# Optimization experiments

Measured on AMD Instinct MI355X. Metric: run time of the kernel, lower is better.

## Reference

```python
import jax, jax.numpy as jnp
import numpy as np

BETA = 0.25


def setup_inputs() -> dict:
    key = jax.random.key(0)
    k1, k2 = jax.random.split(key)
    x = jax.random.normal(k1, (32, 64, 64, 64), dtype=jnp.float32)   # [B, C, H, W]
    emb = jax.random.normal(k2, (1024, 64), dtype=jnp.float32)       # [K, C] codebook
    return {"x": x, "emb": emb}


def reference(x, emb):
    b, c, h, w = x.shape
    # (b h w) c
    z = jnp.transpose(x, (0, 2, 3, 1)).reshape(-1, c)
    # squared euclidean distances (argmin identical to torch.cdist argmin)
    # ||z||^2 - 2 z e^T + ||e||^2, never taking sqrt since only argmin is used
    d = (jnp.sum(z * z, axis=1, keepdims=True)
         - 2.0 * jnp.einsum('nc,kc->nk', z, emb)
         + jnp.sum(emb * emb, axis=1)[None, :])        # [N, K]
    idx = jnp.argmin(d, axis=1)                        # [N] int
    e = emb[idx]                                       # gather [N, C]
    e = jnp.transpose(e.reshape(b, h, w, c), (0, 3, 1, 2))  # [B, C, H, W]
    codebook_loss = jnp.mean((jax.lax.stop_gradient(x) - e) ** 2)
    commitment_loss = BETA * jnp.mean((x - jax.lax.stop_gradient(e)) ** 2)
    loss = codebook_loss + commitment_loss
    o = x + jax.lax.stop_gradient(e - x)               # straight-through
    indices = idx.reshape(b, h, w)
    return (o, loss, indices)
```

## Files before the change

### kernel.cpp

```cpp
#include <hip/hip_runtime.h>

#define BATCH   32
#define CCH     64
#define HW      4096
#define NPIX    (BATCH * HW)
#define KCODES  1024
#define NELEM   (NPIX * CCH)
#define MB      256
#define CK      64
#define MARGIN_Q 3u

typedef _Float16 f16;
typedef __attribute__((ext_vector_type(8))) _Float16 f16x8;
typedef __attribute__((ext_vector_type(4))) float    f32x4;

static __device__ __forceinline__ f32x4 mfma16(f16x8 a, f16x8 b, f32x4 c) {
    return __builtin_amdgcn_mfma_f32_16x16x32_f16(a, b, c, 0, 0, 0);
}

static __device__ __forceinline__ void dma16(void* lds, const void* g) {
    __builtin_amdgcn_global_load_lds(
        (const __attribute__((address_space(1))) unsigned int*)g,
        (__attribute__((address_space(3))) unsigned int*)lds, 16, 0, 0);
}

static __device__ __forceinline__ unsigned med3u(unsigned a, unsigned b, unsigned c) {
    unsigned d;
    asm("v_med3_u32 %0, %1, %2, %3" : "=v"(d) : "v"(a), "v"(b), "v"(c));
    return d;
}

#define WS_EEB_F   64
#define WS_CBH_B   8192
#define WS_CBL_B   139264
#define WS_WL_U    67584

__global__ __launch_bounds__(256) void vq_prep(
    const float* __restrict__ emb, float* __restrict__ wsf,
    unsigned* __restrict__ wsu, f16* __restrict__ cbH, f16* __restrict__ cbL,
    float* __restrict__ eeb_g)
{
    const int t   = threadIdx.x;
    const int gid = blockIdx.x * 256 + t;
    const int row = gid >> 3, gi = gid & 7;
    if (gid == 0) { wsf[0] = 0.f; wsu[1] = 0u; wsu[2] = 0u; }
    const float* src = emb + (size_t)row * CCH + gi * 8;
    float4 v0 = *(const float4*)(src);
    float4 v1 = *(const float4*)(src + 4);
    float vv[8] = {v0.x, v0.y, v0.z, v0.w, v1.x, v1.y, v1.z, v1.w};
    f16x8 h, l;
    float s = 0.f;
#pragma unroll
    for (int j = 0; j < 8; ++j) {
        f16 hh = (f16)vv[j];
        h[j] = hh;
        l[j] = (f16)(vv[j] - (float)hh);
        s = fmaf(vv[j], vv[j], s);
    }
    const int off = row * 64 + 8 * (gi ^ (row & 7));
    *(f16x8*)(cbH + off) = h;
    *(f16x8*)(cbL + off) = l;
    s += __shfl_xor(s, 1, 64);
    s += __shfl_xor(s, 2, 64);
    s += __shfl_xor(s, 4, 64);
    if (gi == 0) eeb_g[row] = fmaf(s, 2048.0f, 1048576.0f);
}

__global__ __launch_bounds__(512, 4) void vq_main(
    const float* __restrict__ x,
    const float* __restrict__ emb,
    const f16* __restrict__ cbH, const f16* __restrict__ cbL,
    const float* __restrict__ eeb_g,
    float* __restrict__ o, float* __restrict__ idx_out,
    float* __restrict__ acc, unsigned* __restrict__ wl_count,
    unsigned* __restrict__ wl, unsigned cap)
{
    __shared__ __align__(16) char smem[32768];
    __shared__ float eebl[2][CK];
    __shared__ unsigned bu1[MB], bu2[MB];
    __shared__ float wred[8];

    const int t    = threadIdx.x;
    const int lane = t & 63;
    const int w    = t >> 6;
    const int col  = lane & 15;
    const int quad = lane >> 4;
    const int c7   = col & 7;
    const int sw0  = 8 * (quad ^ c7);
    const int sw1  = sw0 ^ 32;
    const int n0   = blockIdx.x * MB;
    const int b    = n0 >> 12;
    const int p0   = n0 & 4095;
    const float* xb = x + (size_t)b * (CCH * HW) + p0;

    auto stage = [&](int chunk, int bufi) {
        const int k0 = chunk * CK;
        char* lb = smem + bufi * 16384;
        const char* gH = (const char*)cbH + (size_t)k0 * 128 + w * 1024 + lane * 16;
        const char* gL = (const char*)cbL + (size_t)k0 * 128 + w * 1024 + lane * 16;
        dma16(lb + w * 1024,        gH);
        dma16(lb + 8192 + w * 1024, gL);
        if (t < CK) eebl[bufi][t] = eeb_g[k0 + t];
    };

    stage(0, 0);

    f16x8 aH[2][2], aL[2][2];
#pragma unroll
    for (int rt = 0; rt < 2; ++rt) {
        const int pp = w * 32 + rt * 16 + col;
#pragma unroll
        for (int kc = 0; kc < 2; ++kc) {
            f16x8 h, l;
#pragma unroll
            for (int j = 0; j < 8; ++j) {
                const int c = kc * 32 + quad * 8 + j;
                float zs = -2.0f * xb[(size_t)c * HW + pp];
                f16 hh = (f16)zs;
                h[j] = hh;
                l[j] = (f16)(zs - (float)hh);
            }
            aH[rt][kc] = h;
            aL[rt][kc] = l;
        }
    }

    unsigned best[8], best2[8];
#pragma unroll
    for (int s = 0; s < 8; ++s) { best[s] = 0xFFFFFFFFu; best2[s] = 0xFFFFFFFFu; }

    const f32x4 zero4 = {0.f, 0.f, 0.f, 0.f};

    for (int chunk = 0; chunk < KCODES / CK; ++chunk) {
        const int cur = chunk & 1;
        __syncthreads();
        if (chunk + 1 < KCODES / CK) stage(chunk + 1, cur ^ 1);

        const f16* bufH = (const f16*)(smem + cur * 16384);
        const f16* bufL = bufH + 4096;
        const int k0 = chunk * CK;

#pragma unroll
        for (int tile = 0; tile < CK / 16; ++tile) {
            const f16* bh = bufH + (tile * 16 + col) * 64;
            const f16* bl = bufL + (tile * 16 + col) * 64;
            f16x8 bH0 = *(const f16x8*)(bh + sw0);
            f16x8 bH1 = *(const f16x8*)(bh + sw1);
            f16x8 bL0 = *(const f16x8*)(bl + sw0);
            f16x8 bL1 = *(const f16x8*)(bl + sw1);
            const float eebc = eebl[cur][tile * 16 + col];
            const unsigned kb = (unsigned)(k0 + tile * 16 + col);
#pragma unroll
            for (int rt = 0; rt < 2; ++rt) {
                f32x4 a4 = mfma16(aH[rt][0], bH0, zero4);
                a4 = mfma16(aH[rt][1], bH1, a4);
                a4 = mfma16(aL[rt][0], bH0, a4);
                a4 = mfma16(aL[rt][1], bH1, a4);
                a4 = mfma16(aH[rt][0], bL0, a4);
                a4 = mfma16(aH[rt][1], bL1, a4);
#pragma unroll
                for (int r = 0; r < 4; ++r) {
                    float uf = fmaf(a4[r], 2048.0f, eebc);
                    unsigned pk = (((unsigned)uf) << 10) | kb;
                    const int s = rt * 4 + r;
                    const unsigned b0 = best[s];
                    best2[s] = med3u(b0, best2[s], pk);
                    best[s]  = min(b0, pk);
                }
            }
        }
    }

#pragma unroll
    for (int d = 1; d < 16; d <<= 1) {
#pragma unroll
        for (int s = 0; s < 8; ++s) {
            unsigned ob  = __shfl_xor(best[s],  d, 64);
            unsigned ob2 = __shfl_xor(best2[s], d, 64);
            best2[s] = min(min(best2[s], ob2), max(best[s], ob));
            best[s]  = min(best[s], ob);
        }
    }
    if (col == 0) {
#pragma unroll
        for (int rt = 0; rt < 2; ++rt)
#pragma unroll
            for (int r = 0; r < 4; ++r) {
                const int pl = w * 32 + rt * 16 + quad * 4 + r;
                bu1[pl] = best[rt * 4 + r];
                bu2[pl] = best2[rt * 4 + r];
            }
    }
    __syncthreads();

    const int pix  = t & 255;
    const int half = t >> 8;
    const unsigned bu = bu1[pix];
    const unsigned bidx = bu & 1023u;
    if (half == 0) {
        idx_out[n0 + t] = (float)bidx;
        const unsigned qg = (bu2[pix] >> 10) - (bu >> 10);
        if (qg < MARGIN_Q) {
            unsigned pos = atomicAdd(wl_count, 1u);
            if (pos < cap) wl[pos] = (unsigned)(n0 + t);
        }
    }
    float ss = 0.f;
    {
        const float4* er4 = (const float4*)(emb + (size_t)bidx * CCH) + half * 8;
        const float* xbt = xb + pix;
        float* ob = o + (size_t)b * (CCH * HW) + p0 + pix;
#pragma unroll
        for (int i = 0; i < 8; ++i) {
            float4 ev = er4[i];
            float evv[4] = {ev.x, ev.y, ev.z, ev.w};
#pragma unroll
            for (int q = 0; q < 4; ++q) {
                const int c = half * 32 + i * 4 + q;
                float xv = xbt[(size_t)c * HW];
                float e  = evv[q];
                ob[(size_t)c * HW] = xv + (e - xv);
                float d = xv - e;
                ss = fmaf(d, d, ss);
            }
        }
    }
    for (int off = 32; off; off >>= 1) ss += __shfl_down(ss, off, 64);
    if (lane == 0) wred[w] = ss;
    __syncthreads();
    if (t == 0) {
        float s2 = 0.f;
#pragma unroll
        for (int q = 0; q < 8; ++q) s2 += wred[q];
        atomicAdd(acc, s2);
    }
}

__global__ __launch_bounds__(256) void vq_refine(
    const float* __restrict__ x, const float* __restrict__ emb,
    float* __restrict__ o, float* __restrict__ idx_out,
    float* __restrict__ acc, const unsigned* __restrict__ wl_count,
    const unsigned* __restrict__ wl, unsigned cap,
    float* __restrict__ loss, unsigned* __restrict__ done)
{
    __shared__ float zsh[CCH];
    __shared__ double rbd[4];
    __shared__ int rbi[4];
    __shared__ int s_pk;
    unsigned cnt = *wl_count; if (cnt > cap) cnt = cap;
    const int t = threadIdx.x;

    for (unsigned i = blockIdx.x; i < cnt; i += gridDim.x) {
        const int n = (int)wl[i];
        const int b = n >> 12, p = n & 4095;
        if (t < CCH) zsh[t] = x[(size_t)b * (CCH * HW) + (size_t)t * HW + p];
        __syncthreads();

        double bd = 1e300; int bi = KCODES;
        for (int j = 0; j < 4; ++j) {
            const int k = t + j * 256;
            const float* er = emb + (size_t)k * CCH;
            double d = 0.0;
#pragma unroll
            for (int c = 0; c < CCH; ++c) {
                double tt = (double)zsh[c] - (double)er[c];
                d = fma(tt, tt, d);
            }
            if (d < bd) { bd = d; bi = k; }
        }
        for (int dlt = 1; dlt < 64; dlt <<= 1) {
            double od = __shfl_xor(bd, dlt, 64);
            int    oi = __shfl_xor(bi, dlt, 64);
            if (od < bd || (od == bd && oi < bi)) { bd = od; bi = oi; }
        }
        const int wv = t >> 6;
        if ((t & 63) == 0) { rbd[wv] = bd; rbi[wv] = bi; }
        __syncthreads();
        if (t == 0) {
            double fb = rbd[0]; int fi = rbi[0];
            for (int q = 1; q < 4; ++q)
                if (rbd[q] < fb || (rbd[q] == fb && rbi[q] < fi)) { fb = rbd[q]; fi = rbi[q]; }
            const int old = (int)idx_out[n];
            if (fi != old) { idx_out[n] = (float)fi; s_pk = (old << 16) | fi; }
            else s_pk = -1;
        }
        __syncthreads();
        const int pk = s_pk;
        if (pk >= 0 && t < CCH) {
            const int old = pk >> 16, fi = pk & 0xFFFF;
            const float xv = zsh[t];
            const float eo = emb[(size_t)old * CCH + t];
            const float en = emb[(size_t)fi  * CCH + t];
            o[(size_t)b * (CCH * HW) + (size_t)t * HW + p] = xv + (en - xv);
            const float dn = xv - en, dd = xv - eo;
            float delta = dn * dn - dd * dd;
            for (int off = 32; off; off >>= 1) delta += __shfl_down(delta, off, 64);
            if (t == 0) atomicAdd(acc, delta);
        }
        __syncthreads();
    }

    __threadfence();
    if (t == 0) {
        unsigned prev = atomicAdd(done, 1u);
        if (prev + 1 == gridDim.x) {
            __threadfence();
            float a = atomicAdd(acc, 0.0f);
            loss[0] = 1.25f * a * (1.0f / (float)NELEM);
        }
    }
}

extern "C" void kernel_launch(void* const* d_in, const int* in_sizes, int n_in,
                              void* d_out, int out_size, void* d_ws, size_t ws_size,
                              hipStream_t stream) {
    const float* x   = (const float*)d_in[0];
    const float* emb = (const float*)d_in[1];
    float*    out = (float*)d_out;
    float*    wsf = (float*)d_ws;
    unsigned* wsu = (unsigned*)d_ws;
    char*     wsb = (char*)d_ws;

    float* o_out    = out;
    float* loss_out = out + NELEM;
    float* idx_out  = out + NELEM + 1;
    float* eeb_g    = wsf + WS_EEB_F;
    f16*   cbH      = (f16*)(wsb + WS_CBH_B);
    f16*   cbL      = (f16*)(wsb + WS_CBL_B);
    unsigned* wl    = wsu + WS_WL_U;
    unsigned cap = 0;
    if (ws_size / 4 > WS_WL_U) {
        size_t c = ws_size / 4 - WS_WL_U;
        cap = (unsigned)(c > NPIX ? NPIX : c);
    }

    vq_prep<<<32, 256, 0, stream>>>(emb, wsf, wsu, cbH, cbL, eeb_g);
    vq_main<<<NPIX / MB, 512, 0, stream>>>(x, emb, cbH, cbL, eeb_g, o_out,
                                           idx_out, wsf, wsu + 1, wl, cap);
    vq_refine<<<512, 256, 0, stream>>>(x, emb, o_out, idx_out, wsf,
                                       wsu + 1, wl, cap, loss_out, wsu + 2);
}
```

Before: 175.6 us.

## Halve pixels per block to raise occupancy and finalize loss in separate kernel

Each vq_main block now handles 128 pixels instead of 256, with each wave processing one 16-row tile instead of two. This halves the A-fragment and best/best2 register state, and the launch bound rises to 8 blocks per CU. The grid doubles, so the codebook is staged through LDS twice as often in total and B-fragment reuse across row tiles is lost. The last-block atomic done-counter in vq_refine is replaced by a tiny separate vq_fin kernel, which adds one extra launch.

```diff
diff --git a/kernel.cpp b/kernel.cpp
--- a/kernel.cpp
+++ b/kernel.cpp
@@ -6,7 +6,7 @@
 #define NPIX    (BATCH * HW)
 #define KCODES  1024
 #define NELEM   (NPIX * CCH)
-#define MB      256
+#define MB      128
 #define CK      64
 #define MARGIN_Q 3u
 
@@ -43,7 +43,7 @@
     const int t   = threadIdx.x;
     const int gid = blockIdx.x * 256 + t;
     const int row = gid >> 3, gi = gid & 7;
-    if (gid == 0) { wsf[0] = 0.f; wsu[1] = 0u; wsu[2] = 0u; }
+    if (gid == 0) { wsf[0] = 0.f; wsu[1] = 0u; }
     const float* src = emb + (size_t)row * CCH + gi * 8;
     float4 v0 = *(const float4*)(src);
     float4 v1 = *(const float4*)(src + 4);
@@ -66,7 +66,7 @@
     if (gi == 0) eeb_g[row] = fmaf(s, 2048.0f, 1048576.0f);
 }
 
-__global__ __launch_bounds__(512, 4) void vq_main(
+__global__ __launch_bounds__(512, 8) void vq_main(
     const float* __restrict__ x,
     const float* __restrict__ emb,
     const f16* __restrict__ cbH, const f16* __restrict__ cbL,
@@ -105,10 +105,9 @@
 
     stage(0, 0);
 
-    f16x8 aH[2][2], aL[2][2];
-#pragma unroll
-    for (int rt = 0; rt < 2; ++rt) {
-        const int pp = w * 32 + rt * 16 + col;
+    f16x8 aH[2], aL[2];
+    {
+        const int pp = w * 16 + col;
 #pragma unroll
         for (int kc = 0; kc < 2; ++kc) {
             f16x8 h, l;
@@ -120,14 +119,14 @@
                 h[j] = hh;
                 l[j] = (f16)(zs - (float)hh);
             }
-            aH[rt][kc] = h;
-            aL[rt][kc] = l;
-        }
-    }
-
-    unsigned best[8], best2[8];
-#pragma unroll
-    for (int s = 0; s < 8; ++s) { best[s] = 0xFFFFFFFFu; best2[s] = 0xFFFFFFFFu; }
+            aH[kc] = h;
+            aL[kc] = l;
+        }
+    }
+
+    unsigned best[4], best2[4];
+#pragma unroll
+    for (int s = 0; s < 4; ++s) { best[s] = 0xFFFFFFFFu; best2[s] = 0xFFFFFFFFu; }
 
     const f32x4 zero4 = {0.f, 0.f, 0.f, 0.f};
 
@@ -150,23 +149,19 @@
             f16x8 bL1 = *(const f16x8*)(bl + sw1);
             const float eebc = eebl[cur][tile * 16 + col];
             const unsigned kb = (unsigned)(k0 + tile * 16 + col);
-#pragma unroll
-            for (int rt = 0; rt < 2; ++rt) {
-                f32x4 a4 = mfma16(aH[rt][0], bH0, zero4);
-                a4 = mfma16(aH[rt][1], bH1, a4);
-                a4 = mfma16(aL[rt][0], bH0, a4);
-                a4 = mfma16(aL[rt][1], bH1, a4);
-                a4 = mfma16(aH[rt][0], bL0, a4);
-                a4 = mfma16(aH[rt][1], bL1, a4);
-#pragma unroll
-                for (int r = 0; r < 4; ++r) {
-                    float uf = fmaf(a4[r], 2048.0f, eebc);
-                    unsigned pk = (((unsigned)uf) << 10) | kb;
-                    const int s = rt * 4 + r;
-                    const unsigned b0 = best[s];
-                    best2[s] = med3u(b0, best2[s], pk);
-                    best[s]  = min(b0, pk);
-                }
+            f32x4 a4 = mfma16(aH[0], bH0, zero4);
+            a4 = mfma16(aH[1], bH1, a4);
+            a4 = mfma16(aL[0], bH0, a4);
+            a4 = mfma16(aL[1], bH1, a4);
+            a4 = mfma16(aH[0], bL0, a4);
+            a4 = mfma16(aH[1], bL1, a4);
+#pragma unroll
+            for (int r = 0; r < 4; ++r) {
+                float uf = fmaf(a4[r], 2048.0f, eebc);
+                unsigned pk = (((unsigned)uf) << 10) | kb;
+                const unsigned b0 = best[r];
+                best2[r] = med3u(b0, best2[r], pk);
+                best[r]  = min(b0, pk);
             }
         }
     }
@@ -174,7 +169,7 @@
 #pragma unroll
     for (int d = 1; d < 16; d <<= 1) {
 #pragma unroll
-        for (int s = 0; s < 8; ++s) {
+        for (int s = 0; s < 4; ++s) {
             unsigned ob  = __shfl_xor(best[s],  d, 64);
             unsigned ob2 = __shfl_xor(best2[s], d, 64);
             best2[s] = min(min(best2[s], ob2), max(best[s], ob));
@@ -183,40 +178,38 @@
     }
     if (col == 0) {
 #pragma unroll
-        for (int rt = 0; rt < 2; ++rt)
-#pragma unroll
-            for (int r = 0; r < 4; ++r) {
-                const int pl = w * 32 + rt * 16 + quad * 4 + r;
-                bu1[pl] = best[rt * 4 + r];
-                bu2[pl] = best2[rt * 4 + r];
-            }
+        for (int r = 0; r < 4; ++r) {
+            const int pl = w * 16 + quad * 4 + r;
+            bu1[pl] = best[r];
+            bu2[pl] = best2[r];
+        }
     }
     __syncthreads();
 
-    const int pix  = t & 255;
-    const int half = t >> 8;
+    const int pix = t & 127;
+    const int qh  = t >> 7;
     const unsigned bu = bu1[pix];
     const unsigned bidx = bu & 1023u;
-    if (half == 0) {
-        idx_out[n0 + t] = (float)bidx;
+    if (qh == 0) {
+        idx_out[n0 + pix] = (float)bidx;
         const unsigned qg = (bu2[pix] >> 10) - (bu >> 10);
         if (qg < MARGIN_Q) {
             unsigned pos = atomicAdd(wl_count, 1u);
-            if (pos < cap) wl[pos] = (unsigned)(n0 + t);
+            if (pos < cap) wl[pos] = (unsigned)(n0 + pix);
         }
     }
     float ss = 0.f;
     {
-        const float4* er4 = (const float4*)(emb + (size_t)bidx * CCH) + half * 8;
+        const float4* er4 = (const float4*)(emb + (size_t)bidx * CCH) + qh * 4;
         const float* xbt = xb + pix;
         float* ob = o + (size_t)b * (CCH * HW) + p0 + pix;
 #pragma unroll
-        for (int i = 0; i < 8; ++i) {
+        for (int i = 0; i < 4; ++i) {
             float4 ev = er4[i];
             float evv[4] = {ev.x, ev.y, ev.z, ev.w};
 #pragma unroll
             for (int q = 0; q < 4; ++q) {
-                const int c = half * 32 + i * 4 + q;
+                const int c = qh * 16 + i * 4 + q;
                 float xv = xbt[(size_t)c * HW];
                 float e  = evv[q];
                 ob[(size_t)c * HW] = xv + (e - xv);
@@ -240,8 +233,7 @@
     const float* __restrict__ x, const float* __restrict__ emb,
     float* __restrict__ o, float* __restrict__ idx_out,
     float* __restrict__ acc, const unsigned* __restrict__ wl_count,
-    const unsigned* __restrict__ wl, unsigned cap,
-    float* __restrict__ loss, unsigned* __restrict__ done)
+    const unsigned* __restrict__ wl, unsigned cap)
 {
     __shared__ float zsh[CCH];
     __shared__ double rbd[4];
@@ -299,16 +291,10 @@
         }
         __syncthreads();
     }
-
-    __threadfence();
-    if (t == 0) {
-        unsigned prev = atomicAdd(done, 1u);
-        if (prev + 1 == gridDim.x) {
-            __threadfence();
-            float a = atomicAdd(acc, 0.0f);
-            loss[0] = 1.25f * a * (1.0f / (float)NELEM);
-        }
-    }
+}
+
+__global__ void vq_fin(const float* __restrict__ acc, float* __restrict__ loss) {
+    *loss = 1.25f * (*acc) * (1.0f / (float)NELEM);
 }
 
 extern "C" void kernel_launch(void* const* d_in, const int* in_sizes, int n_in,
@@ -338,5 +324,6 @@
     vq_main<<<NPIX / MB, 512, 0, stream>>>(x, emb, cbH, cbL, eeb_g, o_out,
                                            idx_out, wsf, wsu + 1, wl, cap);
     vq_refine<<<512, 256, 0, stream>>>(x, emb, o_out, idx_out, wsf,
-                                       wsu + 1, wl, cap, loss_out, wsu + 2);
-}
+                                       wsu + 1, wl, cap);
+    vq_fin<<<1, 1, 0, stream>>>(wsf, loss_out);
+}
```

After: 220.7 us. 25.6% more time.
